# Optimization experiments

Hardware: AMD Instinct MI355X
Metric: run time of the kernel (lower is better)

Reference implementation:

```python
import jax, jax.numpy as jnp
import numpy as np
from jax import lax


def setup_inputs() -> dict:
    key = jax.random.key(0)
    ks = jax.random.split(key, 6)
    B, C, H, W = 8, 128, 64, 64   # C = 2*channel, channel (per-branch) c = 64
    c = C // 2
    return {
        "x_up": jax.random.normal(ks[0], (B, C, H, W), dtype=jnp.float32),
        "x_skip": jax.random.normal(ks[1], (B, C, H, W), dtype=jnp.float32),
        # nn.Linear(c, 2c): weight [out,in], bias [out]
        "kv1_w": jax.random.normal(ks[2], (2 * c, c), dtype=jnp.float32) * 0.05,
        "kv1_b": jnp.zeros((2 * c,), dtype=jnp.float32),
        "kv2_w": jax.random.normal(ks[3], (2 * c, c), dtype=jnp.float32) * 0.05,
        "kv2_b": jnp.zeros((2 * c,), dtype=jnp.float32),
        # Conv2d(2c, 2c, 3, stride 1, pad 1, bias=False), OIHW
        "conv_w": jax.random.normal(ks[4], (C, C, 3, 3), dtype=jnp.float32) * 0.05,
        # BatchNorm2d(2c) in inference form (running stats)
        "bn_gamma": jax.random.normal(ks[5], (C,), dtype=jnp.float32) * 0.1 + 1.0,
        "bn_beta": jnp.zeros((C,), dtype=jnp.float32),
        "bn_mean": jnp.zeros((C,), dtype=jnp.float32),
        "bn_var": jnp.ones((C,), dtype=jnp.float32),
    }


def reference(x_up, x_skip, kv1_w, kv1_b, kv2_w, kv2_b, conv_w,
              bn_gamma, bn_beta, bn_mean, bn_var):
    b, C, h, w = x_up.shape
    c = C // 2
    hw = h * w
    up1, up2 = x_up[:, :c], x_up[:, c:]
    sk1, sk2 = x_skip[:, :c], x_skip[:, c:]

    # ---- spatial attention branch (softmax over last axis, hw x hw) ----
    shortcut1 = up1 + sk1
    u1 = up1.reshape(b, c, hw).transpose(0, 2, 1)   # (b, hw, c)
    s1 = sk1.reshape(b, c, hw).transpose(0, 2, 1)   # (b, hw, c)
    kv = s1 @ kv1_w.T + kv1_b                        # (b, hw, 2c)
    k1, v1 = kv[..., :c], kv[..., c:]
    attn = jax.nn.softmax(jnp.einsum('bnc,bmc->bnm', u1, k1), axis=-1)  # (b, hw, hw)
    sout = jnp.einsum('bnm,bmc->bnc', attn, v1)      # (b, hw, c)
    sout = sout.transpose(0, 2, 1).reshape(b, c, h, w) + shortcut1

    # ---- channel attention branch (softmax over dim=1 of the c x c map) ----
    shortcut2 = up2 + sk2
    u2 = up2.reshape(b, c, hw).transpose(0, 2, 1)    # (b, hw, c)
    s2 = sk2.reshape(b, c, hw).transpose(0, 2, 1)
    kv = s2 @ kv2_w.T + kv2_b                        # (b, hw, 2c)
    k2, v2 = kv[..., :c], kv[..., c:]
    A = jax.nn.softmax(jnp.einsum('bnc,bnd->bcd', u2, k2), axis=1)  # (b, c, c)
    cout = jnp.einsum('bnc,bcd->bnd', v2, A)          # (b, hw, c)
    cout = cout.transpose(0, 2, 1).reshape(b, c, h, w) + shortcut2

    # ---- conv + BN (inference) + ReLU ----
    x = jnp.concatenate([sout, cout], axis=1)         # (b, 2c, h, w)
    y = lax.conv_general_dilated(x, conv_w, (1, 1), 'SAME',
                                 dimension_numbers=('NCHW', 'OIHW', 'NCHW'))
    inv = jax.lax.rsqrt(bn_var + 1e-5)
    y = (y - bn_mean[None, :, None, None]) * (inv * bn_gamma)[None, :, None, None] \
        + bn_beta[None, :, None, None]
    return jax.nn.relu(y)
```

## Files before the change

kernel.cpp:

```cpp
#include <hip/hip_runtime.h>
#include <math.h>

#define HW 4096

typedef __attribute__((ext_vector_type(8))) short bh8;
typedef __attribute__((ext_vector_type(4))) float f32x4;
typedef __attribute__((ext_vector_type(2))) unsigned int u32x2;
typedef unsigned int u32;
typedef unsigned short u16;

__device__ __forceinline__ u16 f2bf(float f) {
  union { float f; u32 u; } v; v.f = f;
  u32 u = v.u;
  return (u16)((u + 0x7FFFu + ((u >> 16) & 1u)) >> 16);
}
__device__ __forceinline__ float bf2f(u16 h) {
  union { u32 u; float f; } v; v.u = ((u32)h) << 16;
  return v.f;
}
__device__ __forceinline__ float ubits2f(u32 u) {
  union { u32 u; float f; } v; v.u = u;
  return v.f;
}
__device__ __forceinline__ u32 cvt_pk_bf16(float lo, float hi) {
  u32 r;
  asm("v_cvt_pk_bf16_f32 %0, %1, %2" : "=v"(r) : "v"(lo), "v"(hi));
  return r;
}
__device__ __forceinline__ float fexp2(float x) {
  float r;
  asm("v_exp_f32 %0, %1" : "=v"(r) : "v"(x));
  return r;
}

__global__ __launch_bounds__(256) void kv_proj(
    const float* __restrict__ xs,
    const float* __restrict__ w1, const float* __restrict__ b1,
    const float* __restrict__ w2, const float* __restrict__ b2,
    u32* __restrict__ Knm, u16* __restrict__ Vcm,
    u16* __restrict__ K2t, u16* __restrict__ V2t,
    const float* __restrict__ cw, const float* __restrict__ gamma,
    const float* __restrict__ beta, const float* __restrict__ mean,
    const float* __restrict__ var, u16* __restrict__ Wg,
    float* __restrict__ shb, float* __restrict__ M) {
  __shared__ __align__(16) u16 XsH[64][72];
  __shared__ __align__(16) u16 XsL[64][72];
  __shared__ u32 LtK[64][33];
  const int bid = blockIdx.x;
  const int b = bid & 7, n0 = (bid >> 3) * 64;
  const int t = threadIdx.x;
  const int wq = t >> 6, lane = t & 63, lq = lane & 15, quad = lane >> 4;
  const float* xsb = xs + (size_t)b * 128 * HW;

  {
    int gid = bid * 256 + t;
    for (int i = gid; i < 147456; i += 131072) {
      int tap = i >> 14, oc = (i >> 7) & 127, ic = i & 127;
      float sc = gamma[oc] * rsqrtf(var[oc] + 1e-5f);
      Wg[i] = f2bf(cw[((size_t)(oc * 128 + ic)) * 9 + tap] * sc);
    }
    if (gid < 128) {
      float sc = gamma[gid] * rsqrtf(var[gid] + 1e-5f);
      shb[gid] = beta[gid] - mean[gid] * sc;
    }
    if (gid < 32768) M[gid] = 0.f;
  }

  for (int br = 0; br < 2; ++br) {
    const float* W = br ? w2 : w1;
    const float* bias = br ? b2 : b1;
    const float* src = xsb + (br ? 64 * HW : 0);

    bh8 wh[2][2], wl[2][2];
#pragma unroll
    for (int jt = 0; jt < 2; ++jt)
#pragma unroll
      for (int s = 0; s < 2; ++s) {
        const float* wr = W + (size_t)(wq * 32 + jt * 16 + lq) * 64 + s * 32 + quad * 8;
        float4 a0 = *(const float4*)wr;
        float4 a1 = *(const float4*)(wr + 4);
        float f[8] = {a0.x, a0.y, a0.z, a0.w, a1.x, a1.y, a1.z, a1.w};
        union { u32 u[4]; bh8 v; } H, L;
#pragma unroll
        for (int p = 0; p < 4; ++p) {
          u32 hp = cvt_pk_bf16(f[2 * p], f[2 * p + 1]);
          float h0 = ubits2f(hp << 16);
          float h1 = ubits2f(hp & 0xFFFF0000u);
          H.u[p] = hp;
          L.u[p] = cvt_pk_bf16(f[2 * p] - h0, f[2 * p + 1] - h1);
        }
        wh[jt][s] = H.v;
        wl[jt][s] = L.v;
      }

    if (br) __syncthreads();
    {
      const int n = t & 63, cg = t >> 6;
#pragma unroll
      for (int s8 = 0; s8 < 8; ++s8) {
        int ch0 = s8 * 8 + cg * 2;
        float f0 = src[(size_t)ch0 * HW + n0 + n];
        float f1 = src[(size_t)(ch0 + 1) * HW + n0 + n];
        u32 hp = cvt_pk_bf16(f0, f1);
        float h0 = ubits2f(hp << 16);
        float h1 = ubits2f(hp & 0xFFFF0000u);
        u32 lp = cvt_pk_bf16(f0 - h0, f1 - h1);
        *(u32*)&XsH[n][ch0] = hp;
        *(u32*)&XsL[n][ch0] = lp;
      }
    }
    __syncthreads();

    f32x4 acc[2][4];
#pragma unroll
    for (int nt = 0; nt < 4; ++nt) {
      const int xr = nt * 16 + lq;
      bh8 xh0 = *(const bh8*)&XsH[xr][quad * 8];
      bh8 xh1 = *(const bh8*)&XsH[xr][32 + quad * 8];
      bh8 xl0 = *(const bh8*)&XsL[xr][quad * 8];
      bh8 xl1 = *(const bh8*)&XsL[xr][32 + quad * 8];
#pragma unroll
      for (int jt = 0; jt < 2; ++jt) {
        f32x4 a = (f32x4)(0.f);
        a = __builtin_amdgcn_mfma_f32_16x16x32_bf16(wh[jt][0], xh0, a, 0, 0, 0);
        a = __builtin_amdgcn_mfma_f32_16x16x32_bf16(wh[jt][1], xh1, a, 0, 0, 0);
        a = __builtin_amdgcn_mfma_f32_16x16x32_bf16(wh[jt][0], xl0, a, 0, 0, 0);
        a = __builtin_amdgcn_mfma_f32_16x16x32_bf16(wh[jt][1], xl1, a, 0, 0, 0);
        a = __builtin_amdgcn_mfma_f32_16x16x32_bf16(wl[jt][0], xh0, a, 0, 0, 0);
        a = __builtin_amdgcn_mfma_f32_16x16x32_bf16(wl[jt][1], xh1, a, 0, 0, 0);
        acc[jt][nt] = a;
      }
    }

    if (br == 0) {
      if (wq < 2) {
#pragma unroll
        for (int jt = 0; jt < 2; ++jt) {
          float4 bv = *(const float4*)&bias[wq * 32 + jt * 16 + quad * 4];
#pragma unroll
          for (int nt = 0; nt < 4; ++nt) {
            f32x4 a = acc[jt][nt];
            LtK[nt * 16 + lq][wq * 16 + jt * 8 + quad * 2] =
                cvt_pk_bf16(a[0] + bv.x, a[1] + bv.y);
            LtK[nt * 16 + lq][wq * 16 + jt * 8 + quad * 2 + 1] =
                cvt_pk_bf16(a[2] + bv.z, a[3] + bv.w);
          }
        }
      } else {
#pragma unroll
        for (int jt = 0; jt < 2; ++jt) {
          float4 bv = *(const float4*)&bias[wq * 32 + jt * 16 + quad * 4];
          float bvv[4] = {bv.x, bv.y, bv.z, bv.w};
#pragma unroll
          for (int nt = 0; nt < 4; ++nt)
#pragma unroll
            for (int r = 0; r < 4; ++r) {
              int ch = (wq - 2) * 32 + jt * 16 + quad * 4 + r;
              Vcm[((size_t)b * 64 + ch) * HW + n0 + nt * 16 + lq] =
                  f2bf(acc[jt][nt][r] + bvv[r]);
            }
        }
      }
      __syncthreads();
#pragma unroll
      for (int p = 0; p < 8; ++p) {
        int idx = p * 256 + t;
        int n = idx >> 5, cc = idx & 31;
        Knm[((size_t)b * HW + n0 + n) * 32 + cc] = LtK[n][cc];
      }
    } else {
      u16* base = (wq < 2) ? (K2t + (size_t)b * 64 * HW) : (V2t + (size_t)b * 64 * HW);
      const int chb = (wq & 1) * 32;
#pragma unroll
      for (int jt = 0; jt < 2; ++jt) {
        float4 bv = *(const float4*)&bias[wq * 32 + jt * 16 + quad * 4];
        float bvv[4] = {bv.x, bv.y, bv.z, bv.w};
#pragma unroll
        for (int nt = 0; nt < 4; ++nt)
#pragma unroll
          for (int r = 0; r < 4; ++r) {
            int ch = chb + jt * 16 + quad * 4 + r;
            base[(size_t)ch * HW + n0 + nt * 16 + lq] =
                f2bf(acc[jt][nt][r] + bvv[r]);
          }
      }
    }
  }
}

__device__ __forceinline__ void attn_step(
    const bh8* kf, const bh8* vf, const bh8 (&qb)[4][2], const bh8 ones,
    f32x4 (&O)[4][4], f32x4 (&Osum)[4]) {
  f32x4 S[2][4];
  __builtin_amdgcn_s_setprio(1);
#pragma unroll
  for (int mt = 0; mt < 2; ++mt)
#pragma unroll
    for (int nt = 0; nt < 4; ++nt) {
      f32x4 a = (f32x4)(0.f);
      a = __builtin_amdgcn_mfma_f32_16x16x32_bf16(kf[mt * 2 + 0], qb[nt][0], a, 0, 0, 0);
      a = __builtin_amdgcn_mfma_f32_16x16x32_bf16(kf[mt * 2 + 1], qb[nt][1], a, 0, 0, 0);
      S[mt][nt] = a;
    }
  __builtin_amdgcn_s_setprio(0);
#pragma unroll
  for (int nt = 0; nt < 4; ++nt) {
    const float c = 17.312340f;
    float e00 = fexp2(S[0][nt][0] - c), e01 = fexp2(S[0][nt][1] - c);
    float e02 = fexp2(S[0][nt][2] - c), e03 = fexp2(S[0][nt][3] - c);
    float e10 = fexp2(S[1][nt][0] - c), e11 = fexp2(S[1][nt][1] - c);
    float e12 = fexp2(S[1][nt][2] - c), e13 = fexp2(S[1][nt][3] - c);
    u32 A = cvt_pk_bf16(e00, e01);
    u32 B = cvt_pk_bf16(e02, e03);
    u32 C = cvt_pk_bf16(e10, e11);
    u32 D = cvt_pk_bf16(e12, e13);
    u32x2 rac = __builtin_amdgcn_permlane32_swap(A, C, 0, 0);
    u32x2 rbd = __builtin_amdgcn_permlane32_swap(B, D, 0, 0);
    u32x2 r02 = __builtin_amdgcn_permlane16_swap(rac.x, rac.y, 0, 0);
    u32x2 r13 = __builtin_amdgcn_permlane16_swap(rbd.x, rbd.y, 0, 0);
    union { u32 u[4]; bh8 v; } pb;
    pb.u[0] = r02.x;
    pb.u[1] = r13.x;
    pb.u[2] = r02.y;
    pb.u[3] = r13.y;
    __builtin_amdgcn_s_setprio(1);
#pragma unroll
    for (int ct = 0; ct < 4; ++ct)
      O[ct][nt] = __builtin_amdgcn_mfma_f32_16x16x32_bf16(vf[ct], pb.v, O[ct][nt], 0, 0, 0);
    Osum[nt] = __builtin_amdgcn_mfma_f32_16x16x32_bf16(ones, pb.v, Osum[nt], 0, 0, 0);
    __builtin_amdgcn_s_setprio(0);
  }
}

#define LOADKV(KB, KF, VF)                                            \
  do {                                                                \
    const int n0_ = (KB) * 128;                                       \
    const u16* kr_ = Kb + (size_t)(n0_ + wb + lq) * 64 + quad * 8;    \
    KF[0] = *(const bh8*)(kr_);                                       \
    KF[1] = *(const bh8*)(kr_ + 32);                                  \
    KF[2] = *(const bh8*)(kr_ + 1024);                                \
    KF[3] = *(const bh8*)(kr_ + 1056);                                \
    const u16* vr_ = Vb + (size_t)lq * HW + n0_ + wb + quad * 8;      \
    VF[0] = *(const bh8*)(vr_);                                       \
    VF[1] = *(const bh8*)(vr_ + 16 * HW);                             \
    VF[2] = *(const bh8*)(vr_ + 32 * HW);                             \
    VF[3] = *(const bh8*)(vr_ + 48 * HW);                             \
  } while (0)

__global__ __launch_bounds__(256, 2) void attn_gram(
    const float* __restrict__ xu, const float* __restrict__ xs,
    const u16* __restrict__ Knm, const u16* __restrict__ Vcm,
    u16* __restrict__ xcat,
    const u16* __restrict__ K2t, float* __restrict__ M) {
  __shared__ __align__(16) u16 SMEM[18432];
  const int bid = blockIdx.x;
  const int b = bid & 7;
  const int x = bid >> 3;
  const int t = threadIdx.x;
  const int wq = t >> 6, lane = t & 63, lq = lane & 15, quad = lane >> 4;

  if (x >= 64) {
    const int chunk = x - 64;
    const int nn = chunk * 128;
    const float* ub = xu + ((size_t)b * 128 + 64) * HW;
    const u16* kb2 = K2t + (size_t)b * 64 * HW;
    f32x4 acc[4];
#pragma unroll
    for (int ct = 0; ct < 4; ++ct) acc[ct] = (f32x4)(0.f);
#pragma unroll
    for (int kc = 0; kc < 4; ++kc) {
      const int nb2 = nn + kc * 32 + quad * 8;
      bh8 kb_ = *(const bh8*)&kb2[(size_t)(wq * 16 + lq) * HW + nb2];
#pragma unroll
      for (int ct = 0; ct < 4; ++ct) {
        const float* ar = ub + (size_t)(ct * 16 + lq) * HW + nb2;
        float4 a0 = *(const float4*)ar;
        float4 a1 = *(const float4*)(ar + 4);
        float f[8] = {a0.x, a0.y, a0.z, a0.w, a1.x, a1.y, a1.z, a1.w};
        union { u32 u[4]; bh8 v; } H, L;
#pragma unroll
        for (int p = 0; p < 4; ++p) {
          u32 hp = cvt_pk_bf16(f[2 * p], f[2 * p + 1]);
          float h0 = ubits2f(hp << 16);
          float h1 = ubits2f(hp & 0xFFFF0000u);
          H.u[p] = hp;
          L.u[p] = cvt_pk_bf16(f[2 * p] - h0, f[2 * p + 1] - h1);
        }
        acc[ct] = __builtin_amdgcn_mfma_f32_16x16x32_bf16(H.v, kb_, acc[ct], 0, 0, 0);
        acc[ct] = __builtin_amdgcn_mfma_f32_16x16x32_bf16(L.v, kb_, acc[ct], 0, 0, 0);
      }
    }
    float* Mb = M + (size_t)b * 4096;
#pragma unroll
    for (int ct = 0; ct < 4; ++ct)
#pragma unroll
      for (int r = 0; r < 4; ++r)
        atomicAdd(&Mb[(ct * 16 + quad * 4 + r) * 64 + wq * 16 + lq], acc[ct][r]);
    return;
  }

  const int q0 = x * 64;
  const int wb = wq * 32;
  const float* xub = xu + (size_t)b * 128 * HW;
  const float* xsb = xs + (size_t)b * 128 * HW;
  const u16* Kb = Knm + (size_t)b * HW * 64;
  const u16* Vb = Vcm + (size_t)b * 64 * HW;

  bh8 qb[4][2];
#pragma unroll
  for (int nt = 0; nt < 4; ++nt)
#pragma unroll
    for (int s = 0; s < 2; ++s)
#pragma unroll
      for (int j = 0; j < 8; ++j) {
        int ch = s * 32 + quad * 8 + j;
        qb[nt][s][j] =
            (short)f2bf(xub[(size_t)ch * HW + q0 + nt * 16 + lq] * 1.44269504f);
      }
  bh8 ones;
#pragma unroll
  for (int j = 0; j < 8; ++j) ones[j] = (short)0x3F80;

  f32x4 O[4][4];
#pragma unroll
  for (int ct = 0; ct < 4; ++ct)
#pragma unroll
    for (int nt = 0; nt < 4; ++nt) O[ct][nt] = (f32x4)(0.f);
  f32x4 Osum[4];
#pragma unroll
  for (int nt = 0; nt < 4; ++nt) Osum[nt] = (f32x4)(0.f);

  bh8 kfa[4], vfa[4], kfb[4], vfb[4];
  LOADKV(0, kfa, vfa);
  for (int kb = 0; kb < 32; kb += 2) {
    LOADKV(kb + 1, kfb, vfb);
    attn_step(kfa, vfa, qb, ones, O, Osum);
    if (kb + 2 < 32) LOADKV(kb + 2, kfa, vfa);
    attn_step(kfb, vfb, qb, ones, O, Osum);
  }

  float* Posc = (float*)SMEM;
  float* Lred = (float*)(SMEM + 17408);
  if (quad == 0) {
#pragma unroll
    for (int nt = 0; nt < 4; ++nt) Lred[(wq * 4 + nt) * 16 + lq] = Osum[nt][0];
  }

  const int q = t & 63, cg = t >> 6;
#pragma unroll
  for (int rh = 0; rh < 2; ++rh) {
    if (rh) __syncthreads();
#pragma unroll
    for (int c2 = 0; c2 < 2; ++c2)
#pragma unroll
      for (int nt = 0; nt < 4; ++nt)
#pragma unroll
        for (int r = 0; r < 4; ++r)
          Posc[(wq * 32 + c2 * 16 + quad * 4 + r) * 68 + nt * 16 + lq] =
              O[rh * 2 + c2][nt][r];
    __syncthreads();
    float li = 0.f;
#pragma unroll
    for (int w2 = 0; w2 < 4; ++w2) li += Lred[w2 * 64 + q];
    float inv = 1.f / li;
    u16 h[8];
#pragma unroll
    for (int i = 0; i < 8; ++i) {
      int chl = cg * 8 + i;
      float s = 0.f;
#pragma unroll
      for (int w2 = 0; w2 < 4; ++w2) s += Posc[(w2 * 32 + chl) * 68 + q];
      int ch = rh * 32 + chl;
      size_t g = (size_t)ch * HW + q0 + q;
      h[i] = f2bf(s * inv + xub[g] + xsb[g]);
    }
    u32 pk[4];
#pragma unroll
    for (int j = 0; j < 4; ++j) pk[j] = (u32)h[2 * j] | ((u32)h[2 * j + 1] << 16);
    u16* ob = xcat + ((size_t)b * HW + q0 + q) * 128 + rh * 32 + cg * 8;
    *(uint4*)ob = make_uint4(pk[0], pk[1], pk[2], pk[3]);
  }
}

__global__ __launch_bounds__(256) void chan_apply(
    const u16* __restrict__ V2t, const float* __restrict__ M,
    const float* __restrict__ xu, const float* __restrict__ xs,
    u16* __restrict__ xcat) {
  __shared__ float Vsm[64][65];
  __shared__ float As[64][65];
  __shared__ float red1[4][64], red2[4][64];
  const int bid = blockIdx.x;
  const int b = bid & 7, n0 = (bid >> 3) * 64, t = threadIdx.x;
  const int lane = t & 63, dg = t >> 6;
  const u16* Vb = V2t + (size_t)b * 64 * HW;
  for (int s = 0; s < 16; ++s) {
    int c = s * 4 + dg;
    Vsm[lane][c] = bf2f(Vb[(size_t)c * HW + n0 + lane]);
  }
  for (int idx = t; idx < 4096; idx += 256) As[idx >> 6][idx & 63] = M[b * 4096 + idx];
  __syncthreads();
  float mx = -1e30f;
#pragma unroll
  for (int i = 0; i < 16; ++i) mx = fmaxf(mx, As[dg * 16 + i][lane]);
  red1[dg][lane] = mx;
  __syncthreads();
  mx = fmaxf(fmaxf(red1[0][lane], red1[1][lane]), fmaxf(red1[2][lane], red1[3][lane]));
  float se = 0.f;
#pragma unroll
  for (int i = 0; i < 16; ++i) {
    float e = __expf(As[dg * 16 + i][lane] - mx);
    As[dg * 16 + i][lane] = e;
    se += e;
  }
  red2[dg][lane] = se;
  __syncthreads();

  float acc[16];
#pragma unroll
  for (int i = 0; i < 16; ++i) acc[i] = 0.f;
  for (int c = 0; c < 64; ++c) {
    float v = Vsm[lane][c];
#pragma unroll
    for (int i = 0; i < 16; ++i) acc[i] = fmaf(v, As[c][dg * 16 + i], acc[i]);
  }
  const float* xub = xu + ((size_t)b * 128 + 64) * HW;
  const float* xsb = xs + ((size_t)b * 128 + 64) * HW;
  const int n = n0 + lane;
  u16 hv[16];
#pragma unroll
  for (int i = 0; i < 16; ++i) {
    int d = dg * 16 + i;
    float sm = red2[0][d] + red2[1][d] + red2[2][d] + red2[3][d];
    hv[i] = f2bf(acc[i] / sm + xub[(size_t)d * HW + n] + xsb[(size_t)d * HW + n]);
  }
  u32 pk[8];
#pragma unroll
  for (int j = 0; j < 8; ++j) pk[j] = (u32)hv[2 * j] | ((u32)hv[2 * j + 1] << 16);
  u16* ob = xcat + ((size_t)b * HW + n) * 128 + 64 + dg * 16;
  *(uint4*)(ob) = make_uint4(pk[0], pk[1], pk[2], pk[3]);
  *(uint4*)(ob + 8) = make_uint4(pk[4], pk[5], pk[6], pk[7]);
}

__global__ __launch_bounds__(512) void conv_mfma(
    const u16* __restrict__ X, const u16* __restrict__ Wg,
    const float* __restrict__ shb, float* __restrict__ out) {
  __shared__ __align__(16) u16 In[4 * 66 * 136];
  __shared__ __align__(16) u16 Wt[2][128 * 136];
  const int bid = blockIdx.x;
  const int b = bid & 7, h0 = (bid >> 3) * 2;
  const int t = threadIdx.x;
  const int wq = t >> 6, lane = t & 63, lq = lane & 15, quad = lane >> 4;
  const int nb = (wq & 1) * 64;
  const int mb = (wq >> 1) * 2;
  const u16* Xb = X + (size_t)b * HW * 128;

  if (t < 128) {
    int ih = t >> 5, iwsel = (t >> 4) & 1, ck = t & 15;
    int iw = iwsel ? 65 : 0;
    *(uint4*)&In[(ih * 66 + iw) * 136 + ck * 8] = make_uint4(0, 0, 0, 0);
  }
  for (int ih = 0; ih < 4; ++ih) {
    int h = h0 - 1 + ih;
    bool ok = (h >= 0 && h < 64);
    const u16* src = Xb + (size_t)h * 64 * 128;
#pragma unroll
    for (int p = 0; p < 2; ++p) {
      int idx = p * 512 + t;
      int row = idx >> 4, ck = idx & 15;
      uint4 d = make_uint4(0, 0, 0, 0);
      if (ok) d = *(const uint4*)(src + (size_t)row * 128 + ck * 8);
      *(uint4*)&In[(ih * 66 + 1 + row) * 136 + ck * 8] = d;
    }
  }
  {
    const u16* src = Wg;
#pragma unroll
    for (int p = 0; p < 4; ++p) {
      int idx = p * 512 + t;
      int oc = idx >> 4, ck = idx & 15;
      uint4 d = *(const uint4*)(src + oc * 128 + ck * 8);
      *(uint4*)&Wt[0][oc * 136 + ck * 8] = d;
    }
  }
  __syncthreads();

  f32x4 acc[2][4];
#pragma unroll
  for (int mt = 0; mt < 2; ++mt)
#pragma unroll
    for (int nt = 0; nt < 4; ++nt) acc[mt][nt] = (f32x4)(0.f);

  for (int tap = 0; tap < 9; ++tap) {
    const int cur = tap & 1;
    if (tap < 8) {
      const u16* src = Wg + (size_t)(tap + 1) * 128 * 128;
#pragma unroll
      for (int p = 0; p < 4; ++p) {
        int idx = p * 512 + t;
        int oc = idx >> 4, ck = idx & 15;
        uint4 d = *(const uint4*)(src + oc * 128 + ck * 8);
        *(uint4*)&Wt[cur ^ 1][oc * 136 + ck * 8] = d;
      }
    }
    const int dh = tap / 3, dw = tap - 3 * dh;
    const u16* Wc = &Wt[cur][0];
#pragma unroll
    for (int c = 0; c < 4; ++c) {
      bh8 bf[4];
#pragma unroll
      for (int nt = 0; nt < 4; ++nt)
        bf[nt] = *(const bh8*)&Wc[(nb + nt * 16 + lq) * 136 + c * 32 + quad * 8];
#pragma unroll
      for (int mt = 0; mt < 2; ++mt) {
        int s = (mb + mt) * 16 + lq;
        int ih = (s >> 6) + dh, iw = (s & 63) + dw;
        bh8 af = *(const bh8*)&In[(ih * 66 + iw) * 136 + c * 32 + quad * 8];
#pragma unroll
        for (int nt = 0; nt < 4; ++nt)
          acc[mt][nt] = __builtin_amdgcn_mfma_f32_16x16x32_bf16(af, bf[nt], acc[mt][nt], 0, 0, 0);
      }
    }
    __syncthreads();
  }

  float shv[4];
#pragma unroll
  for (int nt = 0; nt < 4; ++nt) shv[nt] = shb[nb + nt * 16 + lq];
#pragma unroll
  for (int mt = 0; mt < 2; ++mt) {
    int mtile = mb + mt;
    int h = h0 + (mtile >> 2);
    int w0 = ((mtile & 3) * 16) + quad * 4;
#pragma unroll
    for (int nt = 0; nt < 4; ++nt) {
      int oc = nb + nt * 16 + lq;
      float4 v;
      v.x = fmaxf(acc[mt][nt][0] + shv[nt], 0.f);
      v.y = fmaxf(acc[mt][nt][1] + shv[nt], 0.f);
      v.z = fmaxf(acc[mt][nt][2] + shv[nt], 0.f);
      v.w = fmaxf(acc[mt][nt][3] + shv[nt], 0.f);
      *(float4*)&out[((size_t)b * 128 + oc) * HW + h * 64 + w0] = v;
    }
  }
}

extern "C" void kernel_launch(void* const* d_in, const int* in_sizes, int n_in,
                              void* d_out, int out_size, void* d_ws, size_t ws_size,
                              hipStream_t stream) {
  const float* x_up   = (const float*)d_in[0];
  const float* x_skip = (const float*)d_in[1];
  const float* kv1_w  = (const float*)d_in[2];
  const float* kv1_b  = (const float*)d_in[3];
  const float* kv2_w  = (const float*)d_in[4];
  const float* kv2_b  = (const float*)d_in[5];
  const float* conv_w = (const float*)d_in[6];
  const float* bn_g   = (const float*)d_in[7];
  const float* bn_b   = (const float*)d_in[8];
  const float* bn_m   = (const float*)d_in[9];
  const float* bn_v   = (const float*)d_in[10];
  float* out = (float*)d_out;

  char* ws = (char*)d_ws;
  const size_t XCATB_B = (size_t)8 * HW * 128 * 2;
  const size_t KV16_B  = (size_t)8 * 64 * HW * 2;
  size_t off = 0;
  u16*   xcat = (u16*)(ws + off);   off += XCATB_B;
  u16*   K2t  = (u16*)(ws + off);   off += KV16_B;
  u16*   V2t  = (u16*)(ws + off);   off += KV16_B;
  u32*   Knm  = (u32*)(ws + off);   off += KV16_B;
  u16*   Vcm  = (u16*)(ws + off);   off += KV16_B;
  float* M    = (float*)(ws + off); off += (size_t)8 * 4096 * 4;
  u16*   Wg   = (u16*)(ws + off);   off += (size_t)9 * 128 * 128 * 2;
  float* shb  = (float*)(ws + off); off += 512;

  kv_proj<<<512, 256, 0, stream>>>(x_skip, kv1_w, kv1_b, kv2_w, kv2_b,
                                   Knm, Vcm, K2t, V2t,
                                   conv_w, bn_g, bn_b, bn_m, bn_v, Wg,
                                   shb, M);
  attn_gram<<<768, 256, 0, stream>>>(x_up, x_skip, (const u16*)Knm, Vcm,
                                     xcat, K2t, M);
  chan_apply<<<512, 256, 0, stream>>>(V2t, M, x_up, x_skip, xcat);
  conv_mfma<<<256, 512, 0, stream>>>(xcat, Wg, shb, out);
}
```

Baseline: 207.1 us.

## Fuse channel-attention apply into conv kernel, computing halo rows in shared memory

Removes the separate chan_apply kernel and computes the channel-attention output (softmax of M, V2 times A, plus residual) inside conv_mfma, writing it directly into the shared input tile for the upper 64 channels. This eliminates one kernel launch and the global write and reread of half of xcat. In exchange, each conv block recomputes the softmax and the channel output for its 4 halo rows, so rows are computed redundantly. It also adds shared memory use, which may lower occupancy.

```diff
diff --git a/kernel.cpp b/kernel.cpp
--- a/kernel.cpp
+++ b/kernel.cpp
@@ -382,70 +382,15 @@
   }
 }
 
-__global__ __launch_bounds__(256) void chan_apply(
-    const u16* __restrict__ V2t, const float* __restrict__ M,
-    const float* __restrict__ xu, const float* __restrict__ xs,
-    u16* __restrict__ xcat) {
-  __shared__ float Vsm[64][65];
-  __shared__ float As[64][65];
-  __shared__ float red1[4][64], red2[4][64];
-  const int bid = blockIdx.x;
-  const int b = bid & 7, n0 = (bid >> 3) * 64, t = threadIdx.x;
-  const int lane = t & 63, dg = t >> 6;
-  const u16* Vb = V2t + (size_t)b * 64 * HW;
-  for (int s = 0; s < 16; ++s) {
-    int c = s * 4 + dg;
-    Vsm[lane][c] = bf2f(Vb[(size_t)c * HW + n0 + lane]);
-  }
-  for (int idx = t; idx < 4096; idx += 256) As[idx >> 6][idx & 63] = M[b * 4096 + idx];
-  __syncthreads();
-  float mx = -1e30f;
-#pragma unroll
-  for (int i = 0; i < 16; ++i) mx = fmaxf(mx, As[dg * 16 + i][lane]);
-  red1[dg][lane] = mx;
-  __syncthreads();
-  mx = fmaxf(fmaxf(red1[0][lane], red1[1][lane]), fmaxf(red1[2][lane], red1[3][lane]));
-  float se = 0.f;
-#pragma unroll
-  for (int i = 0; i < 16; ++i) {
-    float e = __expf(As[dg * 16 + i][lane] - mx);
-    As[dg * 16 + i][lane] = e;
-    se += e;
-  }
-  red2[dg][lane] = se;
-  __syncthreads();
-
-  float acc[16];
-#pragma unroll
-  for (int i = 0; i < 16; ++i) acc[i] = 0.f;
-  for (int c = 0; c < 64; ++c) {
-    float v = Vsm[lane][c];
-#pragma unroll
-    for (int i = 0; i < 16; ++i) acc[i] = fmaf(v, As[c][dg * 16 + i], acc[i]);
-  }
-  const float* xub = xu + ((size_t)b * 128 + 64) * HW;
-  const float* xsb = xs + ((size_t)b * 128 + 64) * HW;
-  const int n = n0 + lane;
-  u16 hv[16];
-#pragma unroll
-  for (int i = 0; i < 16; ++i) {
-    int d = dg * 16 + i;
-    float sm = red2[0][d] + red2[1][d] + red2[2][d] + red2[3][d];
-    hv[i] = f2bf(acc[i] / sm + xub[(size_t)d * HW + n] + xsb[(size_t)d * HW + n]);
-  }
-  u32 pk[8];
-#pragma unroll
-  for (int j = 0; j < 8; ++j) pk[j] = (u32)hv[2 * j] | ((u32)hv[2 * j + 1] << 16);
-  u16* ob = xcat + ((size_t)b * HW + n) * 128 + 64 + dg * 16;
-  *(uint4*)(ob) = make_uint4(pk[0], pk[1], pk[2], pk[3]);
-  *(uint4*)(ob + 8) = make_uint4(pk[4], pk[5], pk[6], pk[7]);
-}
-
 __global__ __launch_bounds__(512) void conv_mfma(
     const u16* __restrict__ X, const u16* __restrict__ Wg,
-    const float* __restrict__ shb, float* __restrict__ out) {
+    const float* __restrict__ shb, float* __restrict__ out,
+    const u16* __restrict__ V2t, const float* __restrict__ M,
+    const float* __restrict__ xu, const float* __restrict__ xs) {
   __shared__ __align__(16) u16 In[4 * 66 * 136];
   __shared__ __align__(16) u16 Wt[2][128 * 136];
+  __shared__ float As[64 * 65];
+  __shared__ float red1[8][64], red2[8][64];
   const int bid = blockIdx.x;
   const int b = bid & 7, h0 = (bid >> 3) * 2;
   const int t = threadIdx.x;
@@ -460,18 +405,16 @@
     *(uint4*)&In[(ih * 66 + iw) * 136 + ck * 8] = make_uint4(0, 0, 0, 0);
   }
   for (int ih = 0; ih < 4; ++ih) {
-    int h = h0 - 1 + ih;
-    bool ok = (h >= 0 && h < 64);
-    const u16* src = Xb + (size_t)h * 64 * 128;
-#pragma unroll
-    for (int p = 0; p < 2; ++p) {
-      int idx = p * 512 + t;
-      int row = idx >> 4, ck = idx & 15;
-      uint4 d = make_uint4(0, 0, 0, 0);
-      if (ok) d = *(const uint4*)(src + (size_t)row * 128 + ck * 8);
-      *(uint4*)&In[(ih * 66 + 1 + row) * 136 + ck * 8] = d;
-    }
-  }
+    int hcur = h0 - 1 + ih;
+    bool ok = (hcur >= 0 && hcur < 64);
+    const u16* src = Xb + (size_t)hcur * 64 * 128;
+    int row = t >> 3, ck = t & 7;
+    uint4 d = make_uint4(0, 0, 0, 0);
+    if (ok) d = *(const uint4*)(src + (size_t)row * 128 + ck * 8);
+    *(uint4*)&In[(ih * 66 + 1 + row) * 136 + ck * 8] = d;
+  }
+  for (int idx = t; idx < 4096; idx += 512)
+    As[(idx >> 6) * 65 + (idx & 63)] = M[(size_t)b * 4096 + idx];
   {
     const u16* src = Wg;
 #pragma unroll
@@ -480,6 +423,74 @@
       int oc = idx >> 4, ck = idx & 15;
       uint4 d = *(const uint4*)(src + oc * 128 + ck * 8);
       *(uint4*)&Wt[0][oc * 136 + ck * 8] = d;
+    }
+  }
+  __syncthreads();
+
+  const int dcol = t & 63, dg8 = t >> 6;
+  {
+    float mx = -1e30f;
+#pragma unroll
+    for (int i = 0; i < 8; ++i) mx = fmaxf(mx, As[(dg8 * 8 + i) * 65 + dcol]);
+    red1[dg8][dcol] = mx;
+  }
+  __syncthreads();
+  {
+    float mx = red1[0][dcol];
+#pragma unroll
+    for (int g = 1; g < 8; ++g) mx = fmaxf(mx, red1[g][dcol]);
+    float se = 0.f;
+#pragma unroll
+    for (int i = 0; i < 8; ++i) {
+      float e = __expf(As[(dg8 * 8 + i) * 65 + dcol] - mx);
+      As[(dg8 * 8 + i) * 65 + dcol] = e;
+      se += e;
+    }
+    red2[dg8][dcol] = se;
+  }
+  __syncthreads();
+
+  {
+    const u16* V2b = V2t + (size_t)b * 64 * HW;
+    const float* xub2 = xu + ((size_t)b * 128 + 64) * HW;
+    const float* xsb2 = xs + ((size_t)b * 128 + 64) * HW;
+    const int w = t & 63, dgc = t >> 6;
+    float sminv[8];
+#pragma unroll
+    for (int j = 0; j < 8; ++j) {
+      int d = dgc * 8 + j;
+      float sm = 0.f;
+#pragma unroll
+      for (int g = 0; g < 8; ++g) sm += red2[g][d];
+      sminv[j] = 1.f / sm;
+    }
+    for (int ih = 0; ih < 4; ++ih) {
+      int hcur = h0 - 1 + ih;
+      u32 pk[4] = {0u, 0u, 0u, 0u};
+      if (hcur >= 0 && hcur < 64) {
+        int nsp = hcur * 64 + w;
+        float acc[8];
+#pragma unroll
+        for (int j = 0; j < 8; ++j) acc[j] = 0.f;
+        for (int c = 0; c < 64; ++c) {
+          float v = bf2f(V2b[(size_t)c * HW + nsp]);
+#pragma unroll
+          for (int j = 0; j < 8; ++j)
+            acc[j] = fmaf(v, As[c * 65 + dgc * 8 + j], acc[j]);
+        }
+        u16 hv[8];
+#pragma unroll
+        for (int j = 0; j < 8; ++j) {
+          int d = dgc * 8 + j;
+          hv[j] = f2bf(acc[j] * sminv[j] + xub2[(size_t)d * HW + nsp] +
+                       xsb2[(size_t)d * HW + nsp]);
+        }
+#pragma unroll
+        for (int j = 0; j < 4; ++j)
+          pk[j] = (u32)hv[2 * j] | ((u32)hv[2 * j + 1] << 16);
+      }
+      *(uint4*)&In[(ih * 66 + 1 + w) * 136 + 64 + dgc * 8] =
+          make_uint4(pk[0], pk[1], pk[2], pk[3]);
     }
   }
   __syncthreads();
@@ -579,6 +590,5 @@
                                    shb, M);
   attn_gram<<<768, 256, 0, stream>>>(x_up, x_skip, (const u16*)Knm, Vcm,
                                      xcat, K2t, M);
-  chan_apply<<<512, 256, 0, stream>>>(V2t, M, x_up, x_skip, xcat);
-  conv_mfma<<<256, 512, 0, stream>>>(xcat, Wg, shb, out);
-}
+  conv_mfma<<<256, 512, 0, stream>>>(xcat, Wg, shb, out, V2t, M, x_up, x_skip);
+}
```

After: 210.0 us. About the same (+1.4%).
